# Optimization experiments

Measured on AMD Instinct MI355X. Metric: run time of the kernel, lower is better.

## Reference

```python
import jax, jax.numpy as jnp
import numpy as np

T, B, IN, H, OUT, L = 2048, 128, 64, 128, 32, 2


def setup_inputs() -> dict:
    key = jax.random.key(0)
    ks = jax.random.split(key, 8)
    s_in = 1.0 / np.sqrt(H)  # torch LSTM init scale: U(-1/sqrt(H), 1/sqrt(H))
    inp = {
        "x": jax.random.normal(ks[0], (T, B, IN), dtype=jnp.float32),
        "w_ih0": jax.random.uniform(ks[1], (4 * H, IN), minval=-s_in, maxval=s_in, dtype=jnp.float32),
        "w_hh0": jax.random.uniform(ks[2], (4 * H, H), minval=-s_in, maxval=s_in, dtype=jnp.float32),
        "w_ih1": jax.random.uniform(ks[3], (4 * H, H), minval=-s_in, maxval=s_in, dtype=jnp.float32),
        "w_hh1": jax.random.uniform(ks[4], (4 * H, H), minval=-s_in, maxval=s_in, dtype=jnp.float32),
        "fc_w": jax.random.uniform(ks[5], (OUT, H), minval=-s_in, maxval=s_in, dtype=jnp.float32),
        "fc_b": jax.random.uniform(ks[6], (OUT,), minval=-s_in, maxval=s_in, dtype=jnp.float32),
    }
    return inp


def _lstm_layer(x, w_ih, w_hh):
    # x: [T, B, D]; gate order i, f, g, o (PyTorch convention), no bias.
    x_proj = jnp.einsum("tbd,gd->tbg", x, w_ih)  # [T, B, 4H] precomputed input GEMM
    h0 = jnp.zeros((x.shape[1], H), dtype=x.dtype)
    c0 = jnp.zeros((x.shape[1], H), dtype=x.dtype)

    def step(carry, xp):
        h, c = carry
        gates = xp + h @ w_hh.T  # [B, 4H]
        i, f, g, o = jnp.split(gates, 4, axis=-1)
        i = jax.nn.sigmoid(i)
        f = jax.nn.sigmoid(f)
        g = jnp.tanh(g)
        o = jax.nn.sigmoid(o)
        c = f * c + i * g
        h = o * jnp.tanh(c)
        return (h, c), h

    (h_n, c_n), ys = jax.lax.scan(step, (h0, c0), x_proj)
    return ys, h_n, c_n


def reference(x, w_ih0, w_hh0, w_ih1, w_hh1, fc_w, fc_b):
    y0, h0n, c0n = _lstm_layer(x, w_ih0, w_hh0)
    y1, h1n, c1n = _lstm_layer(y0, w_ih1, w_hh1)
    out = jnp.einsum("tbh,oh->tbo", y1, fc_w) + fc_b  # [T, B, OUT]
    h_n = jnp.stack([h0n, h1n], axis=0)  # [L, B, H]
    c_n = jnp.stack([c0n, c1n], axis=0)
    return out, (h_n, c_n)
```

## Files before the change

### kernel.cpp

```cpp
#include <hip/hip_runtime.h>

#define T_ 2048
#define B_ 128
#define IN_ 64
#define H_ 128
#define OUT_ 32
#define CH_ 32
#define RING_ 2

typedef _Float16 half8 __attribute__((ext_vector_type(8)));
typedef _Float16 half4v __attribute__((ext_vector_type(4)));
typedef float float4v __attribute__((ext_vector_type(4)));

#define XSTR 144
#define HSTR 272
#define GRP_ELEMS ((size_t)RING_ * CH_ * 16 * 128)
#define RING_BYTES ((size_t)8 * GRP_ELEMS * 2)

#define NLOG2E  (-1.4426950408889634f)
#define C2LOG2E ( 2.8853900817779268f)

__device__ __forceinline__ float exp2_hw(float x) {
#if __has_builtin(__builtin_amdgcn_exp2f)
  return __builtin_amdgcn_exp2f(x);
#else
  return exp2f(x);
#endif
}
__device__ __forceinline__ float sigm_pre(float xs) {
  return __builtin_amdgcn_rcpf(1.0f + exp2_hw(xs));
}
__device__ __forceinline__ float tanh_pre(float xs) {
  return fmaf(-2.0f, __builtin_amdgcn_rcpf(1.0f + exp2_hw(xs)), 1.0f);
}
__device__ __forceinline__ float tanh_c(float x) { return tanh_pre(x * C2LOG2E); }

__device__ __forceinline__ float4v sigm4(float4v a) {
  float4v r;
#pragma unroll
  for (int i = 0; i < 4; ++i) r[i] = sigm_pre(a[i]);
  return r;
}
__device__ __forceinline__ float4v tanh4(float4v a) {
  float4v r;
#pragma unroll
  for (int i = 0; i < 4; ++i) r[i] = tanh_pre(a[i]);
  return r;
}

__device__ __forceinline__ void bar_light() {
  __builtin_amdgcn_sched_barrier(0);
  asm volatile("s_waitcnt lgkmcnt(0)" ::: "memory");
  __builtin_amdgcn_s_barrier();
  asm volatile("" ::: "memory");
  __builtin_amdgcn_sched_barrier(0);
}
__device__ __forceinline__ void bar_full() {
  __builtin_amdgcn_sched_barrier(0);
  asm volatile("s_waitcnt vmcnt(0) lgkmcnt(0)" ::: "memory");
  __builtin_amdgcn_s_barrier();
  asm volatile("" ::: "memory");
  __builtin_amdgcn_sched_barrier(0);
}

__device__ __forceinline__ half8 make_afrag(const float* __restrict__ W, int K, int row, int col, float sc) {
  const float* p = W + (size_t)row * K + col;
  float4 a = *(const float4*)p;
  float4 b = *(const float4*)(p + 4);
  half8 h;
  h[0]=(_Float16)(a.x*sc); h[1]=(_Float16)(a.y*sc); h[2]=(_Float16)(a.z*sc); h[3]=(_Float16)(a.w*sc);
  h[4]=(_Float16)(b.x*sc); h[5]=(_Float16)(b.y*sc); h[6]=(_Float16)(b.z*sc); h[7]=(_Float16)(b.w*sc);
  return h;
}

__device__ __forceinline__ void wait_ge(int* p, int want) {
  while (__hip_atomic_load(p, __ATOMIC_RELAXED, __HIP_MEMORY_SCOPE_AGENT) < want)
    __builtin_amdgcn_s_sleep(2);
}

__global__ void ring_init(int* f) { if (threadIdx.x < 16) f[threadIdx.x] = 0; }

__global__ __launch_bounds__(512) void lstm_wavefront(
    const float* __restrict__ x, const float* __restrict__ w_ih0,
    const float* __restrict__ w_hh0, const float* __restrict__ w_ih1,
    const float* __restrict__ w_hh1, const float* __restrict__ fc_w,
    const float* __restrict__ fc_b, float* __restrict__ out, char* __restrict__ ws)
{
  const int tid  = threadIdx.x, lane = tid & 63, w = tid >> 6;
  const int quad = lane >> 4, n = lane & 15;
  const int g = blockIdx.x & 7, layer = blockIdx.x >> 3;
  _Float16* ring = (_Float16*)ws + (size_t)g * GRP_ELEMS;
  int* flag     = (int*)(ws + RING_BYTES) + g;
  int* consumed = (int*)(ws + RING_BYTES) + 8 + g;

  __shared__ char sh_x[4 * 16 * XSTR];
  __shared__ char sh_h[2 * 16 * HSTR];

  const size_t hn_base = (size_t)T_ * B_ * OUT_;
  float4v c = {0.f, 0.f, 0.f, 0.f};
  float hf[4] = {0.f, 0.f, 0.f, 0.f};

  for (int i = tid; i < 2 * 16 * HSTR / 4; i += 512) ((unsigned*)sh_h)[i] = 0u;

  if (layer == 0) {
    half8 a_x[4][2], a_h[4][4];
#pragma unroll
    for (int gt = 0; gt < 4; ++gt) {
      const float sc = (gt == 2) ? C2LOG2E : NLOG2E;
      const int row = gt * H_ + w * 16 + n;
#pragma unroll
      for (int kt = 0; kt < 2; ++kt) a_x[gt][kt] = make_afrag(w_ih0, IN_, row, kt * 32 + quad * 8, sc);
#pragma unroll
      for (int kt = 0; kt < 4; ++kt) a_h[gt][kt] = make_afrag(w_hh0, H_, row, kt * 32 + quad * 8, sc);
    }
    const int xn = tid >> 5, xk = (tid & 31) * 2;
#pragma unroll
    for (int k = 0; k < 2; ++k) {
      float2 xv = *(const float2*)(x + ((size_t)k * B_ + g * 16 + xn) * IN_ + xk);
      _Float16* d = (_Float16*)(sh_x + k * 16 * XSTR + xn * XSTR + xk * 2);
      d[0] = (_Float16)xv.x; d[1] = (_Float16)xv.y;
    }
    __syncthreads();
    half4v hh_def = {0, 0, 0, 0};

    for (int t = 0; t < T_; ++t) {
      const int ck = t >> 5, s = t & (CH_ - 1);
      if (s == 0 && ck >= RING_) wait_ge(consumed, ck - 1);
      if (t > 0)
        *(half4v*)(ring + ((size_t)((t - 1) & 63) * 16 + n) * 128 + w * 16 + quad * 4) = hh_def;
      float2 xv = make_float2(0.f, 0.f);
      if (t + 2 < T_) xv = *(const float2*)(x + ((size_t)(t + 2) * B_ + g * 16 + xn) * IN_ + xk);

      half8 Bx[2], Bh[4];
#pragma unroll
      for (int kt = 0; kt < 2; ++kt)
        Bx[kt] = *(const half8*)(sh_x + (t & 3) * 16 * XSTR + n * XSTR + (kt * 32 + quad * 8) * 2);
#pragma unroll
      for (int kt = 0; kt < 4; ++kt)
        Bh[kt] = *(const half8*)(sh_h + (t & 1) * 16 * HSTR + n * HSTR + (kt * 32 + quad * 8) * 2);

      float4v acc[4];
#pragma unroll
      for (int gt = 0; gt < 4; ++gt) acc[gt] = (float4v){0.f, 0.f, 0.f, 0.f};
#pragma unroll
      for (int kt = 0; kt < 2; ++kt)
#pragma unroll
        for (int gt = 0; gt < 4; ++gt)
          acc[gt] = __builtin_amdgcn_mfma_f32_16x16x32_f16(a_x[gt][kt], Bx[kt], acc[gt], 0, 0, 0);
#pragma unroll
      for (int kt = 0; kt < 4; ++kt)
#pragma unroll
        for (int gt = 0; gt < 4; ++gt)
          acc[gt] = __builtin_amdgcn_mfma_f32_16x16x32_f16(a_h[gt][kt], Bh[kt], acc[gt], 0, 0, 0);
      float4v ga[4];
#pragma unroll
      for (int gt = 0; gt < 4; ++gt) ga[gt] = (gt == 2) ? tanh4(acc[gt]) : sigm4(acc[gt]);

      half4v hh;
#pragma unroll
      for (int r = 0; r < 4; ++r) {
        c[r] = fmaf(ga[1][r], c[r], ga[0][r] * ga[2][r]);
        hf[r] = ga[3][r] * tanh_c(c[r]);
        hh[r] = (_Float16)hf[r];
      }
      *(half4v*)(sh_h + ((t & 1) ^ 1) * 16 * HSTR + n * HSTR + (w * 16 + quad * 4) * 2) = hh;
      hh_def = hh;
      if (t + 2 < T_) {
        _Float16* d = (_Float16*)(sh_x + ((t + 2) & 3) * 16 * XSTR + xn * XSTR + xk * 2);
        d[0] = (_Float16)xv.x; d[1] = (_Float16)xv.y;
      }
      if (s == 0) bar_full(); else bar_light();
      if (tid == 0 && s == 0 && t > 0) {
        __builtin_amdgcn_fence(__ATOMIC_RELEASE, "agent");
        __hip_atomic_store(flag, ck, __ATOMIC_RELAXED, __HIP_MEMORY_SCOPE_AGENT);
      }
    }
    *(half4v*)(ring + ((size_t)((T_ - 1) & 63) * 16 + n) * 128 + w * 16 + quad * 4) = hh_def;
    bar_full();
    if (tid == 0) {
      __builtin_amdgcn_fence(__ATOMIC_RELEASE, "agent");
      __hip_atomic_store(flag, T_ / CH_, __ATOMIC_RELAXED, __HIP_MEMORY_SCOPE_AGENT);
    }
    {
      float* hn = out + hn_base;
      float* cn = out + hn_base + 2 * (size_t)B_ * H_;
      size_t idx = (size_t)(g * 16 + n) * H_ + w * 16 + quad * 4;
      *(float4*)(hn + idx) = make_float4(hf[0], hf[1], hf[2], hf[3]);
      *(float4*)(cn + idx) = make_float4(c[0], c[1], c[2], c[3]);
    }
  } else {
    half8 a_i[4][4], a_h[4][4], a_fc[4];
#pragma unroll
    for (int gt = 0; gt < 4; ++gt) {
      const float sc = (gt == 2) ? C2LOG2E : NLOG2E;
      const int row = gt * H_ + w * 16 + n;
#pragma unroll
      for (int kt = 0; kt < 4; ++kt) {
        a_i[gt][kt] = make_afrag(w_ih1, H_, row, kt * 32 + quad * 8, sc);
        a_h[gt][kt] = make_afrag(w_hh1, H_, row, kt * 32 + quad * 8, sc);
      }
    }
    float4 fb = make_float4(0.f, 0.f, 0.f, 0.f);
    if (w < 2) {
#pragma unroll
      for (int kt = 0; kt < 4; ++kt) a_fc[kt] = make_afrag(fc_w, H_, w * 16 + n, kt * 32 + quad * 8, 1.0f);
      fb = *(const float4*)(fc_b + w * 16 + quad * 4);
    }
    __syncthreads();
    half8 By[4];

    for (int t = 0; t < T_; ++t) {
      const int ck = t >> 5, s = t & (CH_ - 1);
      if (s == 0) {
        wait_ge(flag, ck + 1);
        __builtin_amdgcn_fence(__ATOMIC_ACQUIRE, "agent");
        const _Float16* yp = ring + ((size_t)(t & 63) * 16 + n) * 128 + quad * 8;
#pragma unroll
        for (int kt = 0; kt < 4; ++kt) By[kt] = *(const half8*)(yp + kt * 32);
      }
      half8 Bh[4];
#pragma unroll
      for (int kt = 0; kt < 4; ++kt)
        Bh[kt] = *(const half8*)(sh_h + (t & 1) * 16 * HSTR + n * HSTR + (kt * 32 + quad * 8) * 2);
      if (w < 2 && t > 0) {
        float4v af0 = {0.f, 0.f, 0.f, 0.f}, af1 = {0.f, 0.f, 0.f, 0.f};
        af0 = __builtin_amdgcn_mfma_f32_16x16x32_f16(a_fc[0], Bh[0], af0, 0, 0, 0);
        af1 = __builtin_amdgcn_mfma_f32_16x16x32_f16(a_fc[1], Bh[1], af1, 0, 0, 0);
        af0 = __builtin_amdgcn_mfma_f32_16x16x32_f16(a_fc[2], Bh[2], af0, 0, 0, 0);
        af1 = __builtin_amdgcn_mfma_f32_16x16x32_f16(a_fc[3], Bh[3], af1, 0, 0, 0);
        float* op = out + ((size_t)(t - 1) * B_ + g * 16 + n) * OUT_ + w * 16 + quad * 4;
        *(float4*)op = make_float4(af0[0] + af1[0] + fb.x, af0[1] + af1[1] + fb.y,
                                   af0[2] + af1[2] + fb.z, af0[3] + af1[3] + fb.w);
      }
      float4v acc[4];
#pragma unroll
      for (int gt = 0; gt < 4; ++gt) acc[gt] = (float4v){0.f, 0.f, 0.f, 0.f};
#pragma unroll
      for (int kt = 0; kt < 4; ++kt)
#pragma unroll
        for (int gt = 0; gt < 4; ++gt)
          acc[gt] = __builtin_amdgcn_mfma_f32_16x16x32_f16(a_i[gt][kt], By[kt], acc[gt], 0, 0, 0);
#pragma unroll
      for (int kt = 0; kt < 4; ++kt)
#pragma unroll
        for (int gt = 0; gt < 4; ++gt)
          acc[gt] = __builtin_amdgcn_mfma_f32_16x16x32_f16(a_h[gt][kt], Bh[kt], acc[gt], 0, 0, 0);
      float4v ga[4];
#pragma unroll
      for (int gt = 0; gt < 4; ++gt) ga[gt] = (gt == 2) ? tanh4(acc[gt]) : sigm4(acc[gt]);

      half8 Byn[4];
      const bool pf = (s != CH_ - 1) && (t + 1 < T_);
      if (pf) {
        const _Float16* yp = ring + ((size_t)((t + 1) & 63) * 16 + n) * 128 + quad * 8;
#pragma unroll
        for (int kt = 0; kt < 4; ++kt) Byn[kt] = *(const half8*)(yp + kt * 32);
      }
      half4v hh;
#pragma unroll
      for (int r = 0; r < 4; ++r) {
        c[r] = fmaf(ga[1][r], c[r], ga[0][r] * ga[2][r]);
        hf[r] = ga[3][r] * tanh_c(c[r]);
        hh[r] = (_Float16)hf[r];
      }
      *(half4v*)(sh_h + ((t & 1) ^ 1) * 16 * HSTR + n * HSTR + (w * 16 + quad * 4) * 2) = hh;
      bar_light();
      if (s == CH_ - 1 && tid == 0) {
        __builtin_amdgcn_fence(__ATOMIC_RELEASE, "agent");
        __hip_atomic_store(consumed, ck + 1, __ATOMIC_RELAXED, __HIP_MEMORY_SCOPE_AGENT);
      }
      if (pf) {
#pragma unroll
        for (int kt = 0; kt < 4; ++kt) By[kt] = Byn[kt];
      }
    }
    if (w < 2) {
      float4v af = {0.f, 0.f, 0.f, 0.f};
#pragma unroll
      for (int kt = 0; kt < 4; ++kt) {
        half8 Bh = *(const half8*)(sh_h + (T_ & 1) * 16 * HSTR + n * HSTR + (kt * 32 + quad * 8) * 2);
        af = __builtin_amdgcn_mfma_f32_16x16x32_f16(a_fc[kt], Bh, af, 0, 0, 0);
      }
      float* op = out + ((size_t)(T_ - 1) * B_ + g * 16 + n) * OUT_ + w * 16 + quad * 4;
      *(float4*)op = make_float4(af[0] + fb.x, af[1] + fb.y, af[2] + fb.z, af[3] + fb.w);
    }
    {
      float* hn = out + hn_base + (size_t)B_ * H_;
      float* cn = out + hn_base + 3 * (size_t)B_ * H_;
      size_t idx = (size_t)(g * 16 + n) * H_ + w * 16 + quad * 4;
      *(float4*)(hn + idx) = make_float4(hf[0], hf[1], hf[2], hf[3]);
      *(float4*)(cn + idx) = make_float4(c[0], c[1], c[2], c[3]);
    }
  }
}

extern "C" void kernel_launch(void* const* d_in, const int* in_sizes, int n_in,
                              void* d_out, int out_size, void* d_ws, size_t ws_size,
                              hipStream_t stream) {
  const float* x     = (const float*)d_in[0];
  const float* w_ih0 = (const float*)d_in[1];
  const float* w_hh0 = (const float*)d_in[2];
  const float* w_ih1 = (const float*)d_in[3];
  const float* w_hh1 = (const float*)d_in[4];
  const float* fc_w  = (const float*)d_in[5];
  const float* fc_b  = (const float*)d_in[6];
  char* ws = (char*)d_ws;
  ring_init<<<1, 64, 0, stream>>>((int*)(ws + RING_BYTES));
  lstm_wavefront<<<16, 512, 0, stream>>>(x, w_ih0, w_hh0, w_ih1, w_hh1,
                                         fc_w, fc_b, (float*)d_out, ws);
}
```

Measured before the change: 2.906 ms.

## Precompute next step's input-projection MFMAs off the recurrent critical path

```diff
diff --git a/kernel.cpp b/kernel.cpp
--- a/kernel.cpp
+++ b/kernel.cpp
@@ -121,6 +121,20 @@
       d[0] = (_Float16)xv.x; d[1] = (_Float16)xv.y;
     }
     __syncthreads();
+    float4v xacc[4];
+    {
+      half8 Bx[2];
+#pragma unroll
+      for (int kt = 0; kt < 2; ++kt)
+        Bx[kt] = *(const half8*)(sh_x + n * XSTR + (kt * 32 + quad * 8) * 2);
+#pragma unroll
+      for (int gt = 0; gt < 4; ++gt) xacc[gt] = (float4v){0.f, 0.f, 0.f, 0.f};
+#pragma unroll
+      for (int kt = 0; kt < 2; ++kt)
+#pragma unroll
+        for (int gt = 0; gt < 4; ++gt)
+          xacc[gt] = __builtin_amdgcn_mfma_f32_16x16x32_f16(a_x[gt][kt], Bx[kt], xacc[gt], 0, 0, 0);
+    }
     half4v hh_def = {0, 0, 0, 0};
 
     for (int t = 0; t < T_; ++t) {
@@ -131,24 +145,16 @@
       float2 xv = make_float2(0.f, 0.f);
       if (t + 2 < T_) xv = *(const float2*)(x + ((size_t)(t + 2) * B_ + g * 16 + xn) * IN_ + xk);
 
-      half8 Bx[2], Bh[4];
-#pragma unroll
-      for (int kt = 0; kt < 2; ++kt)
-        Bx[kt] = *(const half8*)(sh_x + (t & 3) * 16 * XSTR + n * XSTR + (kt * 32 + quad * 8) * 2);
+      half8 Bh[4];
 #pragma unroll
       for (int kt = 0; kt < 4; ++kt)
         Bh[kt] = *(const half8*)(sh_h + (t & 1) * 16 * HSTR + n * HSTR + (kt * 32 + quad * 8) * 2);
-
       float4v acc[4];
 #pragma unroll
-      for (int gt = 0; gt < 4; ++gt) acc[gt] = (float4v){0.f, 0.f, 0.f, 0.f};
-#pragma unroll
-      for (int kt = 0; kt < 2; ++kt)
-#pragma unroll
-        for (int gt = 0; gt < 4; ++gt)
-          acc[gt] = __builtin_amdgcn_mfma_f32_16x16x32_f16(a_x[gt][kt], Bx[kt], acc[gt], 0, 0, 0);
-#pragma unroll
-      for (int kt = 0; kt < 4; ++kt)
+      for (int gt = 0; gt < 4; ++gt)
+        acc[gt] = __builtin_amdgcn_mfma_f32_16x16x32_f16(a_h[gt][0], Bh[0], xacc[gt], 0, 0, 0);
+#pragma unroll
+      for (int kt = 1; kt < 4; ++kt)
 #pragma unroll
         for (int gt = 0; gt < 4; ++gt)
           acc[gt] = __builtin_amdgcn_mfma_f32_16x16x32_f16(a_h[gt][kt], Bh[kt], acc[gt], 0, 0, 0);
@@ -168,6 +174,19 @@
       if (t + 2 < T_) {
         _Float16* d = (_Float16*)(sh_x + ((t + 2) & 3) * 16 * XSTR + xn * XSTR + xk * 2);
         d[0] = (_Float16)xv.x; d[1] = (_Float16)xv.y;
+      }
+      if (t + 1 < T_) {
+        half8 Bxn[2];
+#pragma unroll
+        for (int kt = 0; kt < 2; ++kt)
+          Bxn[kt] = *(const half8*)(sh_x + ((t + 1) & 3) * 16 * XSTR + n * XSTR + (kt * 32 + quad * 8) * 2);
+#pragma unroll
+        for (int gt = 0; gt < 4; ++gt) xacc[gt] = (float4v){0.f, 0.f, 0.f, 0.f};
+#pragma unroll
+        for (int kt = 0; kt < 2; ++kt)
+#pragma unroll
+          for (int gt = 0; gt < 4; ++gt)
+            xacc[gt] = __builtin_amdgcn_mfma_f32_16x16x32_f16(a_x[gt][kt], Bxn[kt], xacc[gt], 0, 0, 0);
       }
       if (s == 0) bar_full(); else bar_light();
       if (tid == 0 && s == 0 && t > 0) {
@@ -207,7 +226,8 @@
       fb = *(const float4*)(fc_b + w * 16 + quad * 4);
     }
     __syncthreads();
-    half8 By[4];
+    half8 Byc[4];
+    float4v yacc[4];
 
     for (int t = 0; t < T_; ++t) {
       const int ck = t >> 5, s = t & (CH_ - 1);
@@ -216,12 +236,25 @@
         __builtin_amdgcn_fence(__ATOMIC_ACQUIRE, "agent");
         const _Float16* yp = ring + ((size_t)(t & 63) * 16 + n) * 128 + quad * 8;
 #pragma unroll
-        for (int kt = 0; kt < 4; ++kt) By[kt] = *(const half8*)(yp + kt * 32);
+        for (int kt = 0; kt < 4; ++kt) Byc[kt] = *(const half8*)(yp + kt * 32);
+#pragma unroll
+        for (int gt = 0; gt < 4; ++gt) yacc[gt] = (float4v){0.f, 0.f, 0.f, 0.f};
+#pragma unroll
+        for (int kt = 0; kt < 4; ++kt)
+#pragma unroll
+          for (int gt = 0; gt < 4; ++gt)
+            yacc[gt] = __builtin_amdgcn_mfma_f32_16x16x32_f16(a_i[gt][kt], Byc[kt], yacc[gt], 0, 0, 0);
       }
       half8 Bh[4];
 #pragma unroll
       for (int kt = 0; kt < 4; ++kt)
         Bh[kt] = *(const half8*)(sh_h + (t & 1) * 16 * HSTR + n * HSTR + (kt * 32 + quad * 8) * 2);
+      const bool pf = (s != CH_ - 1) && (t + 1 < T_);
+      if (pf) {
+        const _Float16* yp = ring + ((size_t)((t + 1) & 63) * 16 + n) * 128 + quad * 8;
+#pragma unroll
+        for (int kt = 0; kt < 4; ++kt) Byc[kt] = *(const half8*)(yp + kt * 32);
+      }
       if (w < 2 && t > 0) {
         float4v af0 = {0.f, 0.f, 0.f, 0.f}, af1 = {0.f, 0.f, 0.f, 0.f};
         af0 = __builtin_amdgcn_mfma_f32_16x16x32_f16(a_fc[0], Bh[0], af0, 0, 0, 0);
@@ -234,14 +267,10 @@
       }
       float4v acc[4];
 #pragma unroll
-      for (int gt = 0; gt < 4; ++gt) acc[gt] = (float4v){0.f, 0.f, 0.f, 0.f};
-#pragma unroll
-      for (int kt = 0; kt < 4; ++kt)
-#pragma unroll
-        for (int gt = 0; gt < 4; ++gt)
-          acc[gt] = __builtin_amdgcn_mfma_f32_16x16x32_f16(a_i[gt][kt], By[kt], acc[gt], 0, 0, 0);
-#pragma unroll
-      for (int kt = 0; kt < 4; ++kt)
+      for (int gt = 0; gt < 4; ++gt)
+        acc[gt] = __builtin_amdgcn_mfma_f32_16x16x32_f16(a_h[gt][0], Bh[0], yacc[gt], 0, 0, 0);
+#pragma unroll
+      for (int kt = 1; kt < 4; ++kt)
 #pragma unroll
         for (int gt = 0; gt < 4; ++gt)
           acc[gt] = __builtin_amdgcn_mfma_f32_16x16x32_f16(a_h[gt][kt], Bh[kt], acc[gt], 0, 0, 0);
@@ -249,13 +278,6 @@
 #pragma unroll
       for (int gt = 0; gt < 4; ++gt) ga[gt] = (gt == 2) ? tanh4(acc[gt]) : sigm4(acc[gt]);
 
-      half8 Byn[4];
-      const bool pf = (s != CH_ - 1) && (t + 1 < T_);
-      if (pf) {
-        const _Float16* yp = ring + ((size_t)((t + 1) & 63) * 16 + n) * 128 + quad * 8;
-#pragma unroll
-        for (int kt = 0; kt < 4; ++kt) Byn[kt] = *(const half8*)(yp + kt * 32);
-      }
       half4v hh;
 #pragma unroll
       for (int r = 0; r < 4; ++r) {
@@ -264,14 +286,19 @@
         hh[r] = (_Float16)hf[r];
       }
       *(half4v*)(sh_h + ((t & 1) ^ 1) * 16 * HSTR + n * HSTR + (w * 16 + quad * 4) * 2) = hh;
+      if (pf) {
+#pragma unroll
+        for (int gt = 0; gt < 4; ++gt) yacc[gt] = (float4v){0.f, 0.f, 0.f, 0.f};
+#pragma unroll
+        for (int kt = 0; kt < 4; ++kt)
+#pragma unroll
+          for (int gt = 0; gt < 4; ++gt)
+            yacc[gt] = __builtin_amdgcn_mfma_f32_16x16x32_f16(a_i[gt][kt], Byc[kt], yacc[gt], 0, 0, 0);
+      }
       bar_light();
       if (s == CH_ - 1 && tid == 0) {
         __builtin_amdgcn_fence(__ATOMIC_RELEASE, "agent");
         __hip_atomic_store(consumed, ck + 1, __ATOMIC_RELAXED, __HIP_MEMORY_SCOPE_AGENT);
-      }
-      if (pf) {
-#pragma unroll
-        for (int kt = 0; kt < 4; ++kt) By[kt] = Byn[kt];
       }
     }
     if (w < 2) {
```

Result: no change. 2.943 ms (+1.3%).
